# Performance work log

Measured on AMD Instinct MI355X. Metric: run time of the kernel, lower is better.

Reference implementation:

```python
import jax, jax.numpy as jnp
import numpy as np

B, C, H, W = 8, 256, 64, 64
GROUPS = 32
EPS = 1e-6


def setup_inputs() -> dict:
    key = jax.random.key(0)
    ks = jax.random.split(key, 8)
    s = 0.02
    return {
        "x": jax.random.normal(ks[0], (B, C, H, W), dtype=jnp.float32),
        "gn_scale": jnp.ones((C,), jnp.float32),
        "gn_bias": jnp.zeros((C,), jnp.float32),
        "wq": jax.random.normal(ks[1], (C, C), jnp.float32) * s,
        "bq": jnp.zeros((C,), jnp.float32),
        "wk": jax.random.normal(ks[2], (C, C), jnp.float32) * s,
        "bk": jnp.zeros((C,), jnp.float32),
        "wv": jax.random.normal(ks[3], (C, C), jnp.float32) * s,
        "bv": jnp.zeros((C,), jnp.float32),
        "wproj": jax.random.normal(ks[4], (C, C), jnp.float32) * s,
        "bproj": jnp.zeros((C,), jnp.float32),
    }


def _group_norm(x, scale, bias):
    b, c, h, w = x.shape
    xg = x.reshape(b, GROUPS, c // GROUPS, h, w)
    mean = xg.mean(axis=(2, 3, 4), keepdims=True)
    var = xg.var(axis=(2, 3, 4), keepdims=True)
    xn = ((xg - mean) * jax.lax.rsqrt(var + EPS)).reshape(b, c, h, w)
    return xn * scale[None, :, None, None] + bias[None, :, None, None]


def _conv1x1(x, w, b):
    # 1x1 conv == channel-mixing matmul: w is [out_ch, in_ch]
    return jnp.einsum("oc,bchw->bohw", w, x) + b[None, :, None, None]


def reference(x, gn_scale, gn_bias, wq, bq, wk, bk, wv, bv, wproj, bproj):
    b, c, h, w = x.shape
    hn = _group_norm(x, gn_scale, gn_bias)
    q = _conv1x1(hn, wq, bq).reshape(b, c, h * w)  # [b,c,n]
    k = _conv1x1(hn, wk, bk).reshape(b, c, h * w)
    v = _conv1x1(hn, wv, bv).reshape(b, c, h * w)
    # scores[b,n,m] = <q[:, :, n], k[:, :, m]> * c^-0.5  (softmax over keys m)
    scale = jnp.asarray(c, x.dtype) ** -0.5
    attn = jax.nn.softmax(jnp.einsum("bcn,bcm->bnm", q, k) * scale, axis=2)
    # h_[b,c,n] = sum_m v[b,c,m] * attn[b,n,m]
    h_ = jnp.einsum("bcm,bnm->bcn", v, attn).reshape(b, c, h, w)
    h_ = _conv1x1(h_, wproj, bproj)
    return x + h_
```

## Files before the change

### kernel.cpp

```cpp
#include <hip/hip_runtime.h>

#define B_ 8
#define C_ 256
#define N_ 4096
#define G_ 32

typedef __bf16 bf16;
typedef __bf16 bf16x8 __attribute__((ext_vector_type(8)));
typedef float f32x4 __attribute__((ext_vector_type(4)));
typedef float f32x16 __attribute__((ext_vector_type(16)));
typedef long i64;
typedef long i64x2 __attribute__((ext_vector_type(2)));
typedef long i64x2a __attribute__((ext_vector_type(2), may_alias));
typedef int i32x8 __attribute__((ext_vector_type(8)));
typedef int i32x8a __attribute__((ext_vector_type(8), may_alias));
typedef unsigned int u32;
typedef unsigned char u8;
typedef unsigned short u16;
typedef unsigned long long u64;

__device__ __forceinline__ f32x4 mfma16(bf16x8 a, bf16x8 b, f32x4 c) {
    return __builtin_amdgcn_mfma_f32_16x16x32_bf16(a, b, c, 0, 0, 0);
}
__device__ __forceinline__ f32x16 mfma_mx(i32x8 a, i32x8 b, f32x16 c) {
    return __builtin_amdgcn_mfma_scale_f32_32x32x64_f8f6f4(
        a, b, c, 0 , 0 , 0, 0x7F7F7F7F, 0, 0x7F7F7F7F);
}

typedef __attribute__((address_space(1))) const void* gas_t;
typedef __attribute__((address_space(3))) void* las_t;
__device__ __forceinline__ void gl2lds16(const void* g, void* l) {
    __builtin_amdgcn_global_load_lds((gas_t)g, (las_t)l, 16, 0, 0);
}

__device__ __forceinline__ float exp2_hw(float x) {
    return __builtin_amdgcn_exp2f(x);
}

__device__ __forceinline__ u32 fp8_fast(float x) {
    union { float f; u32 u; } c;
    c.f = x;
    return ((c.u + 0x00080000u) >> 20) - 960u;
}
__device__ __forceinline__ u32 pk_fp8x4(float a, float b, float c, float d) {
#if __has_builtin(__builtin_amdgcn_cvt_pk_fp8_f32)
    int w = __builtin_amdgcn_cvt_pk_fp8_f32(a, b, 0, false);
    w = __builtin_amdgcn_cvt_pk_fp8_f32(c, d, w, true);
    return (u32)w;
#else
    return (fp8_fast(a) & 0xff) | ((fp8_fast(b) & 0xff) << 8) |
           ((fp8_fast(c) & 0xff) << 16) | (fp8_fast(d) << 24);
#endif
}

__global__ __launch_bounds__(256) void gn_part(const float* __restrict__ x,
                                               float* __restrict__ gpart) {
    int blk = blockIdx.x;
    int b = blk >> 8, g = (blk >> 3) & 31, qe = blk & 7;
    int tid = threadIdx.x;
    int c = g * 8 + (tid >> 5);
    const float* row = x + ((size_t)(b * C_ + c)) * N_ + qe * 512;
    float s = 0.f, s2 = 0.f;
    for (int n = (tid & 31) * 4; n < 512; n += 128) {
        float4 v = *(const float4*)(row + n);
        s += v.x + v.y + v.z + v.w;
        s2 += v.x * v.x + v.y * v.y + v.z * v.z + v.w * v.w;
    }
    for (int off = 32; off; off >>= 1) {
        s += __shfl_xor(s, off);
        s2 += __shfl_xor(s2, off);
    }
    __shared__ float red[8];
    int wid = tid >> 6;
    if ((tid & 63) == 0) { red[wid] = s; red[4 + wid] = s2; }
    __syncthreads();
    if (tid == 0) {
        gpart[blk * 2] = red[0] + red[1] + red[2] + red[3];
        gpart[blk * 2 + 1] = red[4] + red[5] + red[6] + red[7];
    }
}

__global__ __launch_bounds__(256) void gn_apply(const float* __restrict__ x,
                                                const float* __restrict__ gsc,
                                                const float* __restrict__ gbi,
                                                const float* __restrict__ gpart,
                                                bf16* __restrict__ hn) {
    __shared__ float tile[32][33];
    int b = blockIdx.z, c0 = blockIdx.y * 32, n0 = blockIdx.x * 32;
    int tx = threadIdx.x & 31, ty = threadIdx.x >> 5;
    for (int i = 0; i < 4; i++) {
        int cl = ty + i * 8;
        int c = c0 + cl;
        int g = c >> 3;
        const float* gp = gpart + ((size_t)(b * G_ + g)) * 16;
        float S = 0.f, S2 = 0.f;
#pragma unroll
        for (int j = 0; j < 8; j++) { S += gp[j * 2]; S2 += gp[j * 2 + 1]; }
        float mean = S * (1.f / 32768.f);
        float var = S2 * (1.f / 32768.f) - mean * mean;
        float rstd = rsqrtf(var + 1e-6f);
        float sc = gsc[c] * rstd;
        float bs = gbi[c] - mean * sc;
        float v = x[((size_t)(b * C_ + c)) * N_ + n0 + tx];
        tile[cl][tx] = v * sc + bs;
    }
    __syncthreads();
    for (int i = 0; i < 4; i++) {
        int nl = ty + i * 8;
        hn[((size_t)(b * N_ + n0 + nl)) * C_ + c0 + tx] = (bf16)tile[tx][nl];
    }
}

__global__ __launch_bounds__(256) void cvt_w(const float* __restrict__ wq,
                                             const float* __restrict__ wk,
                                             const float* __restrict__ wv,
                                             const float* __restrict__ wp,
                                             bf16* __restrict__ dst) {
    int i = blockIdx.x * 256 + threadIdx.x;
    dst[i] = (bf16)wq[i];
    dst[65536 + i] = (bf16)wk[i];
    dst[131072 + i] = (bf16)wv[i];
    dst[196608 + i] = (bf16)wp[i];
}

__global__ __launch_bounds__(256) void gemm_qkv(const bf16* __restrict__ A,
                                                const bf16* __restrict__ Wq,
                                                const bf16* __restrict__ Wk,
                                                const bf16* __restrict__ Wv,
                                                const float* __restrict__ bq,
                                                const float* __restrict__ bk,
                                                const float* __restrict__ bv,
                                                u8* __restrict__ q8,
                                                u8* __restrict__ k8,
                                                u8* __restrict__ v8) {
    __shared__ __align__(16) bf16 As[64][32];
    __shared__ __align__(16) bf16 Wqs[64][32];
    __shared__ __align__(16) bf16 Wks[64][32];
    __shared__ __align__(16) bf16 Wvs[64][32];
    int m0 = blockIdx.x * 64;
    int n0 = blockIdx.y * 64;
    int tid = threadIdx.x;
    int wv_ = tid >> 6, lane = tid & 63, lr = lane & 15, lq = lane >> 4;
    int wm = (wv_ & 1) * 32, wn = (wv_ >> 1) * 32;
    int sr = tid >> 2, sk = (tid & 3) * 8;
    f32x4 qacc[2][2] = {}, kacc[2][2] = {}, vacc[2][2] = {};
    for (int kk = 0; kk < C_; kk += 32) {
        __syncthreads();
        gl2lds16(&A[(size_t)(m0 + sr) * C_ + kk + sk], &As[sr][sk]);
        gl2lds16(&Wq[(size_t)(n0 + sr) * C_ + kk + sk], &Wqs[sr][sk]);
        gl2lds16(&Wk[(size_t)(n0 + sr) * C_ + kk + sk], &Wks[sr][sk]);
        gl2lds16(&Wv[(size_t)(n0 + sr) * C_ + kk + sk], &Wvs[sr][sk]);
        __syncthreads();
        bf16x8 a0 = *(const bf16x8*)&As[wm + lr][lq * 8];
        bf16x8 a1 = *(const bf16x8*)&As[wm + 16 + lr][lq * 8];
        bf16x8 q0 = *(const bf16x8*)&Wqs[wn + lr][lq * 8];
        bf16x8 q1 = *(const bf16x8*)&Wqs[wn + 16 + lr][lq * 8];
        bf16x8 k0 = *(const bf16x8*)&Wks[wn + lr][lq * 8];
        bf16x8 k1 = *(const bf16x8*)&Wks[wn + 16 + lr][lq * 8];
        bf16x8 v0 = *(const bf16x8*)&Wvs[wn + lr][lq * 8];
        bf16x8 v1 = *(const bf16x8*)&Wvs[wn + 16 + lr][lq * 8];
        qacc[0][0] = mfma16(a0, q0, qacc[0][0]);
        qacc[0][1] = mfma16(a0, q1, qacc[0][1]);
        qacc[1][0] = mfma16(a1, q0, qacc[1][0]);
        qacc[1][1] = mfma16(a1, q1, qacc[1][1]);
        kacc[0][0] = mfma16(a0, k0, kacc[0][0]);
        kacc[0][1] = mfma16(a0, k1, kacc[0][1]);
        kacc[1][0] = mfma16(a1, k0, kacc[1][0]);
        kacc[1][1] = mfma16(a1, k1, kacc[1][1]);
        vacc[0][0] = mfma16(a0, v0, vacc[0][0]);
        vacc[0][1] = mfma16(a0, v1, vacc[0][1]);
        vacc[1][0] = mfma16(a1, v0, vacc[1][0]);
        vacc[1][1] = mfma16(a1, v1, vacc[1][1]);
    }
    for (int i = 0; i < 2; i++)
        for (int j = 0; j < 2; j++) {
            int col = n0 + wn + j * 16 + lr;
            float bvq = bq[col], bvk = bk[col], bvv = bv[col];
            u32 qw = pk_fp8x4(qacc[i][j][0] + bvq, qacc[i][j][1] + bvq,
                              qacc[i][j][2] + bvq, qacc[i][j][3] + bvq);
            u32 kw = pk_fp8x4(kacc[i][j][0] + bvk, kacc[i][j][1] + bvk,
                              kacc[i][j][2] + bvk, kacc[i][j][3] + bvk);
            u32 vw = pk_fp8x4(vacc[i][j][0] + bvv, vacc[i][j][1] + bvv,
                              vacc[i][j][2] + bvv, vacc[i][j][3] + bvv);
            for (int r = 0; r < 4; r++) {
                int row = m0 + wm + i * 16 + lq * 4 + r;
                q8[(size_t)row * C_ + col] = (u8)(qw >> (8 * r));
                k8[(size_t)row * C_ + col] = (u8)(kw >> (8 * r));
                int bb = row >> 12, n = row & (N_ - 1);
                int h = (n >> 11) & 1, mtl = (n >> 6) & 31, k6 = n & 63;
                int hbv = (k6 >> 2) & 1;
                int jv = ((k6 >> 5) << 4) | (((k6 >> 3) & 3) << 2) | (k6 & 3);
                v8[((size_t)(((bb * 2 + h) * 32 + mtl) * 2 + hbv)) * 8192 +
                   col * 32 + jv] = (u8)(vw >> (8 * r));
            }
        }
}

__global__ __launch_bounds__(128, 2) void attn(const u8* __restrict__ q,
                                               const u8* __restrict__ k,
                                               const u8* __restrict__ vT,
                                               bf16* __restrict__ O0,
                                               bf16* __restrict__ O1,
                                               float* __restrict__ lp) {
    __shared__ __align__(16) u8 smem[24576];

    int flat = blockIdx.x + (blockIdx.y << 6) + (blockIdx.z << 7);
    int nid = (flat & 7) * 128 + (flat >> 3);
    int q0 = (nid & 63) * 64;
    int h = (nid >> 6) & 1;
    int b = nid >> 7;
    int tid = threadIdx.x;
    int w = tid >> 6, lane = tid & 63, lc = lane & 31, hb = lane >> 5;

    const u8* kglob = k + ((size_t)(b * N_) + h * 2048) * 256;
    const u8* vglob = vT + ((size_t)(b * 2 + h)) * 32 * 16384 + hb * 8192 + lc * 32;

    u32 offK[4];
#pragma unroll
    for (int j = 0; j < 4; j++) {
        int p = j * 128 + tid;
        offK[j] = (u32)((p >> 4) * 256 + (((p & 15) ^ ((p >> 4) & 15)) << 4));
    }

    const u8* qrow = q + ((size_t)(b * N_ + q0 + w * 32 + lc)) * 256 + hb * 32;
    i32x8 qf[4];
#pragma unroll
    for (int kh = 0; kh < 4; kh++) qf[kh] = *(const i32x8a*)&qrow[kh * 64];

    f32x16 oacc[8] = {};
    f32x16 eacc = {};
    u32 swz = (u32)(lc & 15);

    auto STAGE_K = [&](int sidx, int buf) {
        const u8* kg = kglob + (size_t)sidx * 8192;
        u8* dst = smem + buf * 8192;
#pragma unroll
        for (int j = 0; j < 4; j++)
            gl2lds16(kg + offK[j], dst + (j * 128 + tid) * 16);
    };

    STAGE_K(0, 0);
    STAGE_K(1, 1);

    i32x8 pfA = {};
    for (int mt = 0; mt < 32; mt++) {
        int bufa = (2 * mt) % 3, bufb = (2 * mt + 1) % 3, bufc = (2 * mt + 2) % 3;
        if (mt < 31) {
            STAGE_K(2 * mt + 2, bufc);
            asm volatile("s_waitcnt vmcnt(4)" ::: "memory");
        } else {
            asm volatile("s_waitcnt vmcnt(0)" ::: "memory");
        }
        __builtin_amdgcn_s_barrier();

        const u8* Ka = smem + bufa * 8192;
        const u8* Kb = smem + bufb * 8192;
        __builtin_amdgcn_s_setprio(1);

        f32x16 st0 = {}, st1 = {};
#pragma unroll
        for (int kh = 0; kh < 4; kh++) {
            u32 g0 = (u32)(kh * 4 + hb * 2);
            union { i64x2 h2[2]; i32x8 v; } kf0, kf1;
            kf0.h2[0] = *(const i64x2a*)&Ka[lc * 256 + ((g0 ^ swz) << 4)];
            kf0.h2[1] = *(const i64x2a*)&Ka[lc * 256 + (((g0 + 1) ^ swz) << 4)];
            st0 = mfma_mx(kf0.v, qf[kh], st0);
            kf1.h2[0] = *(const i64x2a*)&Kb[lc * 256 + ((g0 ^ swz) << 4)];
            kf1.h2[1] = *(const i64x2a*)&Kb[lc * 256 + (((g0 + 1) ^ swz) << 4)];
            st1 = mfma_mx(kf1.v, qf[kh], st1);
        }

        if (mt) {
            const u8* Vb = vglob + (size_t)(mt - 1) * 16384;
            i32x8 vr[8];
#pragma unroll
            for (int ct = 0; ct < 8; ct++) vr[ct] = *(const i32x8a*)&Vb[ct * 1024];
#pragma unroll
            for (int ct = 0; ct < 8; ct++)
                oacc[ct] = mfma_mx(pfA, vr[ct], oacc[ct]);
        }

        f32x16 e0, e1;
#pragma unroll
        for (int i = 0; i < 16; i++) {
            e0[i] = exp2_hw(st0[i] * (1.44269504089f * 0.0625f));
            e1[i] = exp2_hw(st1[i] * (1.44269504089f * 0.0625f));
        }
        eacc += e0;
        eacc += e1;
#pragma unroll
        for (int t4 = 0; t4 < 4; t4++) {
            pfA[t4] = (int)pk_fp8x4(e0[t4 * 4], e0[t4 * 4 + 1], e0[t4 * 4 + 2],
                                    e0[t4 * 4 + 3]);
            pfA[4 + t4] = (int)pk_fp8x4(e1[t4 * 4], e1[t4 * 4 + 1], e1[t4 * 4 + 2],
                                        e1[t4 * 4 + 3]);
        }
        __builtin_amdgcn_s_setprio(0);

        if (mt < 31) {
            asm volatile("s_waitcnt lgkmcnt(0)" ::: "memory");
            __builtin_amdgcn_s_barrier();
            STAGE_K(2 * mt + 3, bufa);
        }
    }

    {
        const u8* Vb = vglob + (size_t)31 * 16384;
#pragma unroll
        for (int ct = 0; ct < 8; ct++) {
            i32x8 vf = *(const i32x8a*)&Vb[ct * 1024];
            oacc[ct] = mfma_mx(pfA, vf, oacc[ct]);
        }
    }

    float hs = 0.f;
#pragma unroll
    for (int i = 0; i < 16; i++) hs += eacc[i];
    float lsum = hs + __shfl_xor(hs, 32);

    bf16* Op = h ? O1 : O0;
#pragma unroll
    for (int ct = 0; ct < 8; ct++)
#pragma unroll
        for (int r = 0; r < 16; r++) {
            int qq = (r & 3) + hb * 4 + (r >> 2) * 8;
            Op[((size_t)(b * N_ + q0 + w * 32 + qq)) * C_ + ct * 32 + lc] =
                (bf16)oacc[ct][r];
        }
    if (hb == 0)
        lp[((size_t)(h * B_ + b)) * N_ + q0 + w * 32 + lc] = lsum;
}

__global__ __launch_bounds__(256) void proj_res(const bf16* __restrict__ W,
                                                const bf16* __restrict__ O0,
                                                const bf16* __restrict__ O1,
                                                const float* __restrict__ lp,
                                                const float* __restrict__ bias,
                                                const float* __restrict__ x,
                                                float* __restrict__ out) {
    __shared__ __align__(16) bf16 Ws[256][32];
    __shared__ __align__(16) bf16 As[64][32];
    int n0 = blockIdx.x * 64;
    int tid = threadIdx.x;
    int wv_ = tid >> 6, lane = tid & 63, lr = lane & 15, lq = lane >> 4;
    int wm = (wv_ & 1) * 32;
    int wn = (wv_ >> 1) * 32;
    int sr = tid >> 2, sk = (tid & 3) * 8;
    int T = n0 + sr, bb = T >> 12, nn = T & (N_ - 1);
    float inv = 1.f / (lp[(size_t)bb * N_ + nn] + lp[(size_t)(B_ + bb) * N_ + nn]);
    f32x4 acc[4][2][2] = {};
    for (int kk = 0; kk < C_; kk += 32) {
        __syncthreads();
#pragma unroll
        for (int p = 0; p < 4; p++)
            gl2lds16(&W[(size_t)(p * 64 + sr) * C_ + kk + sk], &Ws[p * 64 + sr][sk]);
        bf16x8 o0 = *(const bf16x8*)&O0[(size_t)T * C_ + kk + sk];
        bf16x8 o1 = *(const bf16x8*)&O1[(size_t)T * C_ + kk + sk];
        bf16x8 cm;
#pragma unroll
        for (int e = 0; e < 8; e++) cm[e] = (bf16)(((float)o0[e] + (float)o1[e]) * inv);
        *(bf16x8*)&As[sr][sk] = cm;
        __syncthreads();
        bf16x8 a0 = *(const bf16x8*)&As[wm + lr][lq * 8];
        bf16x8 a1 = *(const bf16x8*)&As[wm + 16 + lr][lq * 8];
#pragma unroll
        for (int ot = 0; ot < 4; ot++) {
            bf16x8 w0 = *(const bf16x8*)&Ws[ot * 64 + wn + lr][lq * 8];
            bf16x8 w1 = *(const bf16x8*)&Ws[ot * 64 + wn + 16 + lr][lq * 8];
            acc[ot][0][0] = mfma16(w0, a0, acc[ot][0][0]);
            acc[ot][0][1] = mfma16(w0, a1, acc[ot][0][1]);
            acc[ot][1][0] = mfma16(w1, a0, acc[ot][1][0]);
            acc[ot][1][1] = mfma16(w1, a1, acc[ot][1][1]);
        }
    }
#pragma unroll
    for (int ot = 0; ot < 4; ot++)
        for (int i = 0; i < 2; i++)
            for (int j = 0; j < 2; j++) {
                int Tt = n0 + wm + j * 16 + lr;
                int b = Tt >> 12, n = Tt & (N_ - 1);
                for (int r = 0; r < 4; r++) {
                    int o = ot * 64 + wn + i * 16 + lq * 4 + r;
                    size_t idx = ((size_t)(b * C_ + o)) * N_ + n;
                    out[idx] = x[idx] + acc[ot][i][j][r] + bias[o];
                }
            }
}

extern "C" void kernel_launch(void* const* d_in, const int* in_sizes, int n_in,
                              void* d_out, int out_size, void* d_ws, size_t ws_size,
                              hipStream_t stream) {
    const float* x = (const float*)d_in[0];
    const float* gsc = (const float*)d_in[1];
    const float* gbi = (const float*)d_in[2];
    const float* wq = (const float*)d_in[3];
    const float* bq = (const float*)d_in[4];
    const float* wk = (const float*)d_in[5];
    const float* bk = (const float*)d_in[6];
    const float* wv = (const float*)d_in[7];
    const float* bv = (const float*)d_in[8];
    const float* wp = (const float*)d_in[9];
    const float* bp = (const float*)d_in[10];
    float* out = (float*)d_out;

    const size_t SZ = (size_t)B_ * N_ * C_;
    char* ws = (char*)d_ws;
    bf16* wb = (bf16*)(ws + 4096);
    char* base = ws + 4096 + 524288;
    bf16* hn = (bf16*)base;
    u8* q8 = (u8*)(base + SZ * 2);
    u8* k8 = (u8*)(base + SZ * 3);
    u8* v8 = (u8*)(base + SZ * 4);
    bf16* O0 = (bf16*)base;
    bf16* O1 = (bf16*)(base + SZ * 5);
    float* gpart = (float*)(base + SZ * 7);
    float* lpart = (float*)(base + SZ * 7);

    cvt_w<<<256, 256, 0, stream>>>(wq, wk, wv, wp, wb);
    gn_part<<<B_ * G_ * 8, 256, 0, stream>>>(x, gpart);
    gn_apply<<<dim3(N_ / 32, C_ / 32, B_), 256, 0, stream>>>(x, gsc, gbi, gpart, hn);
    gemm_qkv<<<dim3(B_ * N_ / 64, C_ / 64), 256, 0, stream>>>(
        hn, wb, wb + 65536, wb + 131072, bq, bk, bv, q8, k8, v8);
    attn<<<dim3(N_ / 64, 2, B_), 128, 0, stream>>>(q8, k8, v8, O0, O1, lpart);
    proj_res<<<B_ * N_ / 64, 256, 0, stream>>>(
        wb + 196608, O0, O1, lpart, bp, x, out);
}
```

Measured before the change: 305.0 us.

## Stage V through LDS and double the attention block's query rows

```diff
diff --git a/kernel.cpp b/kernel.cpp
--- a/kernel.cpp
+++ b/kernel.cpp
@@ -190,36 +190,39 @@
                 int h = (n >> 11) & 1, mtl = (n >> 6) & 31, k6 = n & 63;
                 int hbv = (k6 >> 2) & 1;
                 int jv = ((k6 >> 5) << 4) | (((k6 >> 3) & 3) << 2) | (k6 & 3);
+                jv ^= ((col ^ hbv) & 1) << 4;
                 v8[((size_t)(((bb * 2 + h) * 32 + mtl) * 2 + hbv)) * 8192 +
                    col * 32 + jv] = (u8)(vw >> (8 * r));
             }
         }
 }
 
-__global__ __launch_bounds__(128, 2) void attn(const u8* __restrict__ q,
+__global__ __launch_bounds__(256, 2) void attn(const u8* __restrict__ q,
                                                const u8* __restrict__ k,
                                                const u8* __restrict__ vT,
                                                bf16* __restrict__ O0,
                                                bf16* __restrict__ O1,
                                                float* __restrict__ lp) {
-    __shared__ __align__(16) u8 smem[24576];
-
-    int flat = blockIdx.x + (blockIdx.y << 6) + (blockIdx.z << 7);
-    int nid = (flat & 7) * 128 + (flat >> 3);
-    int q0 = (nid & 63) * 64;
-    int h = (nid >> 6) & 1;
-    int b = nid >> 7;
+    __shared__ __align__(16) u8 smem[65536];
+
+    int flat = blockIdx.x;
+    int nid = (flat & 7) * 64 + (flat >> 3);
+    int q0 = (nid & 31) * 128;
+    int h = (nid >> 5) & 1;
+    int b = nid >> 6;
     int tid = threadIdx.x;
     int w = tid >> 6, lane = tid & 63, lc = lane & 31, hb = lane >> 5;
 
     const u8* kglob = k + ((size_t)(b * N_) + h * 2048) * 256;
-    const u8* vglob = vT + ((size_t)(b * 2 + h)) * 32 * 16384 + hb * 8192 + lc * 32;
-
-    u32 offK[4];
+    const u8* vglob = vT + ((size_t)(b * 2 + h)) * 32 * 16384;
+
+    u32 offK[4], lin[4];
 #pragma unroll
     for (int j = 0; j < 4; j++) {
-        int p = j * 128 + tid;
-        offK[j] = (u32)((p >> 4) * 256 + (((p & 15) ^ ((p >> 4) & 15)) << 4));
+        int p = j * 256 + tid;
+        int rK = p >> 4;
+        offK[j] = (u32)(rK * 256 + (((p & 15) ^ (rK & 15)) << 4));
+        lin[j] = (u32)(p << 4);
     }
 
     const u8* qrow = q + ((size_t)(b * N_ + q0 + w * 32 + lc)) * 256 + hb * 32;
@@ -229,35 +232,23 @@
 
     f32x16 oacc[8] = {};
     f32x16 eacc = {};
+    i32x8 pfA = {};
     u32 swz = (u32)(lc & 15);
-
-    auto STAGE_K = [&](int sidx, int buf) {
-        const u8* kg = kglob + (size_t)sidx * 8192;
-        u8* dst = smem + buf * 8192;
-#pragma unroll
-        for (int j = 0; j < 4; j++)
-            gl2lds16(kg + offK[j], dst + (j * 128 + tid) * 16);
+    u32 vsw0 = (u32)(((lc ^ hb) & 1) << 4);
+
+    auto STAGE_KP = [&](int mt, u32 koff) {
+        const u8* kg = kglob + (size_t)mt * 16384;
+#pragma unroll
+        for (int j = 0; j < 4; j++) gl2lds16(kg + offK[j], smem + koff + lin[j]);
     };
-
-    STAGE_K(0, 0);
-    STAGE_K(1, 1);
-
-    i32x8 pfA = {};
-    for (int mt = 0; mt < 32; mt++) {
-        int bufa = (2 * mt) % 3, bufb = (2 * mt + 1) % 3, bufc = (2 * mt + 2) % 3;
-        if (mt < 31) {
-            STAGE_K(2 * mt + 2, bufc);
-            asm volatile("s_waitcnt vmcnt(4)" ::: "memory");
-        } else {
-            asm volatile("s_waitcnt vmcnt(0)" ::: "memory");
-        }
-        __builtin_amdgcn_s_barrier();
-
-        const u8* Ka = smem + bufa * 8192;
-        const u8* Kb = smem + bufb * 8192;
-        __builtin_amdgcn_s_setprio(1);
-
-        f32x16 st0 = {}, st1 = {};
+    auto STAGE_V = [&](int mt, u32 voff) {
+        const u8* vg = vglob + (size_t)mt * 16384;
+#pragma unroll
+        for (int j = 0; j < 4; j++) gl2lds16(vg + lin[j], smem + voff + lin[j]);
+    };
+    auto QKT = [&](u32 koff, f32x16& st0, f32x16& st1) {
+        const u8* Ka = smem + koff;
+        const u8* Kb = smem + koff + 8192;
 #pragma unroll
         for (int kh = 0; kh < 4; kh++) {
             u32 g0 = (u32)(kh * 4 + hb * 2);
@@ -269,17 +260,18 @@
             kf1.h2[1] = *(const i64x2a*)&Kb[lc * 256 + (((g0 + 1) ^ swz) << 4)];
             st1 = mfma_mx(kf1.v, qf[kh], st1);
         }
-
-        if (mt) {
-            const u8* Vb = vglob + (size_t)(mt - 1) * 16384;
-            i32x8 vr[8];
-#pragma unroll
-            for (int ct = 0; ct < 8; ct++) vr[ct] = *(const i32x8a*)&Vb[ct * 1024];
-#pragma unroll
-            for (int ct = 0; ct < 8; ct++)
-                oacc[ct] = mfma_mx(pfA, vr[ct], oacc[ct]);
-        }
-
+    };
+    auto PV = [&](u32 voff, i32x8 pf) {
+#pragma unroll
+        for (int ct = 0; ct < 8; ct++) {
+            u32 base = voff + (u32)(hb * 8192 + (ct * 32 + lc) * 32);
+            union { i64x2 h2[2]; i32x8 v; } vf;
+            vf.h2[0] = *(const i64x2a*)&smem[base + vsw0];
+            vf.h2[1] = *(const i64x2a*)&smem[base + (vsw0 ^ 16)];
+            oacc[ct] = mfma_mx(pf, vf.v, oacc[ct]);
+        }
+    };
+    auto SM = [&](const f32x16& st0, const f32x16& st1) {
         f32x16 e0, e1;
 #pragma unroll
         for (int i = 0; i < 16; i++) {
@@ -295,23 +287,46 @@
             pfA[4 + t4] = (int)pk_fp8x4(e1[t4 * 4], e1[t4 * 4 + 1], e1[t4 * 4 + 2],
                                         e1[t4 * 4 + 3]);
         }
+    };
+
+    STAGE_KP(0, 0);
+    asm volatile("s_waitcnt vmcnt(0)" ::: "memory");
+    __builtin_amdgcn_s_barrier();
+    STAGE_KP(1, 16384);
+    STAGE_V(0, 32768);
+    {
+        __builtin_amdgcn_s_setprio(1);
+        f32x16 st0 = {}, st1 = {};
+        QKT(0, st0, st1);
+        SM(st0, st1);
         __builtin_amdgcn_s_setprio(0);
-
-        if (mt < 31) {
-            asm volatile("s_waitcnt lgkmcnt(0)" ::: "memory");
-            __builtin_amdgcn_s_barrier();
-            STAGE_K(2 * mt + 3, bufa);
-        }
-    }
-
+    }
+    for (int mt = 1; mt <= 30; ++mt) {
+        asm volatile("s_waitcnt vmcnt(0)" ::: "memory");
+        __builtin_amdgcn_s_barrier();
+        STAGE_KP(mt + 1, (u32)(((mt + 1) & 1) * 16384));
+        STAGE_V(mt, (u32)(32768 + (mt & 1) * 16384));
+        __builtin_amdgcn_s_setprio(1);
+        f32x16 st0 = {}, st1 = {};
+        QKT((u32)((mt & 1) * 16384), st0, st1);
+        PV((u32)(32768 + ((mt - 1) & 1) * 16384), pfA);
+        SM(st0, st1);
+        __builtin_amdgcn_s_setprio(0);
+    }
+    asm volatile("s_waitcnt vmcnt(0)" ::: "memory");
+    __builtin_amdgcn_s_barrier();
+    STAGE_V(31, 32768 + 16384);
     {
-        const u8* Vb = vglob + (size_t)31 * 16384;
-#pragma unroll
-        for (int ct = 0; ct < 8; ct++) {
-            i32x8 vf = *(const i32x8a*)&Vb[ct * 1024];
-            oacc[ct] = mfma_mx(pfA, vf, oacc[ct]);
-        }
-    }
+        __builtin_amdgcn_s_setprio(1);
+        f32x16 st0 = {}, st1 = {};
+        QKT(16384, st0, st1);
+        PV(32768, pfA);
+        SM(st0, st1);
+        __builtin_amdgcn_s_setprio(0);
+    }
+    asm volatile("s_waitcnt vmcnt(0)" ::: "memory");
+    __builtin_amdgcn_s_barrier();
+    PV(32768 + 16384, pfA);
 
     float hs = 0.f;
 #pragma unroll
@@ -421,7 +436,7 @@
     gn_apply<<<dim3(N_ / 32, C_ / 32, B_), 256, 0, stream>>>(x, gsc, gbi, gpart, hn);
     gemm_qkv<<<dim3(B_ * N_ / 64, C_ / 64), 256, 0, stream>>>(
         hn, wb, wb + 65536, wb + 131072, bq, bk, bv, q8, k8, v8);
-    attn<<<dim3(N_ / 64, 2, B_), 128, 0, stream>>>(q8, k8, v8, O0, O1, lpart);
+    attn<<<512, 256, 0, stream>>>(q8, k8, v8, O0, O1, lpart);
     proj_res<<<B_ * N_ / 64, 256, 0, stream>>>(
         wb + 196608, O0, O1, lpart, bp, x, out);
 }
```

Measured after the change: 263.7 us. -13.5%, faster.
